# Kernel tuning notes

Hardware: AMD Instinct MI355X
Metric: run time of the kernel (lower is better)

Reference implementation:

```python
import jax, jax.numpy as jnp
import numpy as np

EMB = 768
HEADS = 12
HD = EMB // HEADS
FF = 4 * EMB
EPS = 1e-5


def gelu_tanh(x):
    c = jnp.sqrt(jnp.asarray(2.0 / jnp.pi, x.dtype))
    return 0.5 * x * (1.0 + jnp.tanh(c * (x + 0.044715 * x ** 3)))


def layernorm(x, scale, shift):
    mean = x.mean(-1, keepdims=True)
    var = ((x - mean) ** 2).mean(-1, keepdims=True)
    return scale * (x - mean) / jnp.sqrt(var + EPS) + shift


def setup_inputs() -> dict:
    key = jax.random.key(0)
    ks = jax.random.split(key, 12)
    s = 0.02
    return {
        "x": jax.random.normal(ks[0], (8, 1024, EMB), jnp.float32),
        "Wq": jax.random.normal(ks[1], (EMB, EMB), jnp.float32) * s,
        "Wk": jax.random.normal(ks[2], (EMB, EMB), jnp.float32) * s,
        "Wv": jax.random.normal(ks[3], (EMB, EMB), jnp.float32) * s,
        "Wo": jax.random.normal(ks[4], (EMB, EMB), jnp.float32) * s,
        "bo": jnp.zeros((EMB,), jnp.float32),
        "W1": jax.random.normal(ks[5], (EMB, FF), jnp.float32) * s,
        "b1": jnp.zeros((FF,), jnp.float32),
        "W2": jax.random.normal(ks[6], (FF, EMB), jnp.float32) * s,
        "b2": jnp.zeros((EMB,), jnp.float32),
        "ln1_scale": jnp.ones((EMB,), jnp.float32),
        "ln1_shift": jnp.zeros((EMB,), jnp.float32),
        "ln2_scale": jnp.ones((EMB,), jnp.float32),
        "ln2_shift": jnp.zeros((EMB,), jnp.float32),
    }


def reference(x, Wq, Wk, Wv, Wo, bo, W1, b1, W2, b2,
              ln1_scale, ln1_shift, ln2_scale, ln2_shift):
    B, T, _ = x.shape
    inp = x
    h = layernorm(x, ln1_scale, ln1_shift)
    # QKV projections (no bias, qkv_bias=False)
    q = (h @ Wq).reshape(B, T, HEADS, HD).transpose(0, 2, 1, 3)  # [B,H,T,hd]
    k = (h @ Wk).reshape(B, T, HEADS, HD).transpose(0, 2, 1, 3)
    v = (h @ Wv).reshape(B, T, HEADS, HD).transpose(0, 2, 1, 3)
    scores = jnp.einsum('bhqd,bhkd->bhqk', q, k)
    causal = jnp.triu(jnp.ones((T, T), bool), k=1)
    scores = jnp.where(causal, -jnp.inf, scores)
    attn = jax.nn.softmax(scores / jnp.sqrt(jnp.asarray(HD, x.dtype)), axis=-1)
    ctx = jnp.einsum('bhqk,bhkd->bhqd', attn, v)
    ctx = ctx.transpose(0, 2, 1, 3).reshape(B, T, EMB)
    attn_out = ctx @ Wo + bo
    x = inp + attn_out  # dropout is identity (rate 0 / eval)
    inp = x
    h = layernorm(x, ln2_scale, ln2_shift)
    ff = gelu_tanh(h @ W1 + b1) @ W2 + b2
    return inp + ff
```

## Files before the change

kernel.cpp:

```cpp
#include <hip/hip_runtime.h>
#include <hip/hip_bf16.h>
#include <stdint.h>
#include <stddef.h>

#define EMB 768
#define FFD 3072
#define NHEAD 12
#define HD 64
#define SEQ 1024
#define NTOK 8192
#define QKVW 2304

typedef unsigned short u16;
typedef __attribute__((ext_vector_type(8))) short short8;
typedef __attribute__((ext_vector_type(4))) float f32x4;

__device__ __forceinline__ u16 f2bf(float f) {
  union { float f; uint32_t u; } w; w.f = f;
  uint32_t x = w.u + 0x7fffu + ((w.u >> 16) & 1u);
  return (u16)(x >> 16);
}

__device__ __forceinline__ float bf2f(uint32_t v) {
  union { uint32_t u; float f; } c; c.u = v << 16; return c.f;
}

__device__ __forceinline__ uint32_t pkbf(float lo, float hi) {
  __hip_bfloat162 h = __float22bfloat162_rn(float2{lo, hi});
  union { __hip_bfloat162 h; uint32_t u; } cv; cv.h = h;
  return cv.u;
}

__device__ __forceinline__ void g2l16(const void* g, void* l) {
  __builtin_amdgcn_global_load_lds(
      (const __attribute__((address_space(1))) void*)g,
      (__attribute__((address_space(3))) void*)l, 16, 0, 0);
}

__global__ __launch_bounds__(256)
void prep_kernel(const float* __restrict__ Wq, const float* __restrict__ Wk,
                 const float* __restrict__ Wv, const float* __restrict__ Wo,
                 const float* __restrict__ W1, const float* __restrict__ W2,
                 u16* __restrict__ qkvT, u16* __restrict__ woT,
                 u16* __restrict__ w1T, u16* __restrict__ w2T,
                 const float* __restrict__ x, const float* __restrict__ sc,
                 const float* __restrict__ sh, u16* __restrict__ h1) {
  __shared__ float tile[32][33];
  const int id = blockIdx.x;
  if (id >= 6912) {
    const int wave = threadIdx.x >> 6, lane = threadIdx.x & 63;
    const int row = (id - 6912) * 4 + wave;
    const float* xr = x + (size_t)row * EMB;
    float4 v[3];
    float s = 0.f, ss = 0.f;
#pragma unroll
    for (int i = 0; i < 3; ++i) {
      v[i] = *(const float4*)(xr + lane * 4 + i * 256);
      s += v[i].x + v[i].y + v[i].z + v[i].w;
      ss += v[i].x * v[i].x + v[i].y * v[i].y + v[i].z * v[i].z + v[i].w * v[i].w;
    }
#pragma unroll
    for (int m = 1; m < 64; m <<= 1) { s += __shfl_xor(s, m, 64); ss += __shfl_xor(ss, m, 64); }
    const float mean = s * (1.f / EMB);
    const float inv = rsqrtf(ss * (1.f / EMB) - mean * mean + 1e-5f);
    u16* orow = h1 + (size_t)row * EMB;
#pragma unroll
    for (int i = 0; i < 3; ++i) {
      const int c = lane * 4 + i * 256;
      const float4 s4 = *(const float4*)(sc + c);
      const float4 h4 = *(const float4*)(sh + c);
      uint2 w2;
      w2.x = pkbf((v[i].x - mean) * inv * s4.x + h4.x, (v[i].y - mean) * inv * s4.y + h4.y);
      w2.y = pkbf((v[i].z - mean) * inv * s4.z + h4.z, (v[i].w - mean) * inv * s4.w + h4.w);
      *(uint2*)(orow + c) = w2;
    }
    return;
  }
  const float* in; u16* out; int K, N, bx, by;
  if (id < 1728) {
    const int z = id / 576, rem = id % 576;
    in = z == 0 ? Wq : (z == 1 ? Wk : Wv);
    out = qkvT + (size_t)z * EMB * EMB;
    K = EMB; N = EMB; bx = rem % 24; by = rem / 24;
  } else if (id < 2304) {
    const int rem = id - 1728;
    in = Wo; out = woT; K = EMB; N = EMB; bx = rem % 24; by = rem / 24;
  } else if (id < 4608) {
    const int rem = id - 2304;
    in = W1; out = w1T; K = EMB; N = FFD; bx = rem % 96; by = rem / 96;
  } else {
    const int rem = id - 4608;
    in = W2; out = w2T; K = FFD; N = EMB; bx = rem % 24; by = rem / 24;
  }
  const int n0 = bx * 32, k0 = by * 32;
  const int tx = threadIdx.x & 31;
  const int ty = threadIdx.x >> 5;
#pragma unroll
  for (int i = 0; i < 32; i += 8)
    tile[ty + i][tx] = in[(size_t)(k0 + ty + i) * N + n0 + tx];
  __syncthreads();
#pragma unroll
  for (int i = 0; i < 32; i += 8)
    out[(size_t)(n0 + ty + i) * K + k0 + tx] = f2bf(tile[tx][ty + i]);
}

__global__ __launch_bounds__(256)
void ln_bf_vec_kernel(const u16* __restrict__ x, const float* __restrict__ sc,
                      const float* __restrict__ sh, u16* __restrict__ out) {
  const int wave = threadIdx.x >> 6, lane = threadIdx.x & 63;
  const int row = blockIdx.x * 4 + wave;
  const u16* xr = x + (size_t)row * EMB;
  float v[3][4];
  float s = 0.f, ss = 0.f;
#pragma unroll
  for (int i = 0; i < 3; ++i) {
    const uint2 r2 = *(const uint2*)(xr + lane * 4 + i * 256);
    v[i][0] = bf2f(r2.x & 0xffffu);
    v[i][1] = bf2f(r2.x >> 16);
    v[i][2] = bf2f(r2.y & 0xffffu);
    v[i][3] = bf2f(r2.y >> 16);
#pragma unroll
    for (int j = 0; j < 4; ++j) { s += v[i][j]; ss += v[i][j] * v[i][j]; }
  }
#pragma unroll
  for (int m = 1; m < 64; m <<= 1) { s += __shfl_xor(s, m, 64); ss += __shfl_xor(ss, m, 64); }
  const float mean = s * (1.f / EMB);
  const float inv = rsqrtf(ss * (1.f / EMB) - mean * mean + 1e-5f);
  u16* orow = out + (size_t)row * EMB;
#pragma unroll
  for (int i = 0; i < 3; ++i) {
    const int c = lane * 4 + i * 256;
    const float4 s4 = *(const float4*)(sc + c);
    const float4 h4 = *(const float4*)(sh + c);
    uint2 w2;
    w2.x = pkbf((v[i][0] - mean) * inv * s4.x + h4.x, (v[i][1] - mean) * inv * s4.y + h4.y);
    w2.y = pkbf((v[i][2] - mean) * inv * s4.z + h4.z, (v[i][3] - mean) * inv * s4.w + h4.w);
    *(uint2*)(orow + c) = w2;
  }
}

template <int EPI, int MT, bool SWAP>
__global__ __launch_bounds__(256, 4)
void gemm_kernel(const u16* __restrict__ A, const u16* __restrict__ BT,
                 void* __restrict__ Cp, const float* __restrict__ bias,
                 const float* __restrict__ res, const u16* __restrict__ res16,
                 u16* __restrict__ vTp, int M, int N, int K) {
  constexpr int MI = MT / 32;
  __shared__ u16 As[MT * 64];
  __shared__ u16 Bs[128 * 64];

  const int nwg = gridDim.x * gridDim.y;
  const int orig = blockIdx.y * gridDim.x + blockIdx.x;
  const int swz = (orig & 7) * (nwg >> 3) + (orig >> 3);
  const int m0 = (swz % gridDim.y) * MT;
  const int n0 = (swz / gridDim.y) * 128;

  const int tid = threadIdx.x;
  const int wave = tid >> 6, lane = tid & 63;
  const int wr = wave >> 1, wc = wave & 1;
  const int r = lane & 15, g = lane >> 4;
  const int lrow = lane >> 3;
  const int lelem = (lane & 7) * 8;

  f32x4 acc[MI][4] = {};

  const int nkt = K >> 6;
  for (int kt = 0; kt < nkt; ++kt) {
    const int k0 = kt << 6;
    if (kt) __syncthreads();
#pragma unroll
    for (int q = 0; q < MT / 32; ++q) {
      const int chunk = q * 4 + wave;
      const int row = chunk * 8 + lrow;
      const int e = lelem ^ ((row & 7) << 3);
      g2l16(A + (size_t)(m0 + row) * K + k0 + e, As + chunk * 512);
    }
#pragma unroll
    for (int q = 0; q < 4; ++q) {
      const int chunk = q * 4 + wave;
      const int row = chunk * 8 + lrow;
      const int e = lelem ^ ((row & 7) << 3);
      g2l16(BT + (size_t)(n0 + row) * K + k0 + e, Bs + chunk * 512);
    }
    __syncthreads();
#pragma unroll
    for (int kk = 0; kk < 2; ++kk) {
      short8 af[MI], bf[4];
#pragma unroll
      for (int mi = 0; mi < MI; ++mi) {
        const int row = wr * (MT / 2) + mi * 16 + r;
        af[mi] = *(const short8*)(As + row * 64 + ((kk * 32 + g * 8) ^ ((row & 7) << 3)));
      }
#pragma unroll
      for (int ni = 0; ni < 4; ++ni) {
        const int row = wc * 64 + ni * 16 + r;
        bf[ni] = *(const short8*)(Bs + row * 64 + ((kk * 32 + g * 8) ^ ((row & 7) << 3)));
      }
#pragma unroll
      for (int mi = 0; mi < MI; ++mi)
#pragma unroll
        for (int ni = 0; ni < 4; ++ni) {
          if constexpr (SWAP)
            acc[mi][ni] = __builtin_amdgcn_mfma_f32_16x16x32_bf16(bf[ni], af[mi], acc[mi][ni], 0, 0, 0);
          else
            acc[mi][ni] = __builtin_amdgcn_mfma_f32_16x16x32_bf16(af[mi], bf[ni], acc[mi][ni], 0, 0, 0);
        }
    }
  }

  if constexpr (!SWAP) {
#pragma unroll
    for (int mi = 0; mi < MI; ++mi)
#pragma unroll
      for (int ni = 0; ni < 4; ++ni) {
        const int rowb = m0 + wr * (MT / 2) + mi * 16 + 4 * g;
        const int col = n0 + wc * 64 + ni * 16 + r;
        u16 pk[4];
#pragma unroll
        for (int j = 0; j < 4; ++j) pk[j] = f2bf(acc[mi][ni][j]);
        if (col < 1536) {
#pragma unroll
          for (int j = 0; j < 4; ++j)
            ((u16*)Cp)[(size_t)(rowb + j) * N + col] = pk[j];
        } else {
          uint2 w2;
          w2.x = (uint32_t)pk[0] | ((uint32_t)pk[1] << 16);
          w2.y = (uint32_t)pk[2] | ((uint32_t)pk[3] << 16);
          *(uint2*)(vTp + (size_t)(col - 1536) * NTOK + rowb) = w2;
        }
      }
  } else {
#pragma unroll
    for (int mi = 0; mi < MI; ++mi) {
      const int m = m0 + wr * (MT / 2) + mi * 16 + r;
#pragma unroll
      for (int ni = 0; ni < 4; ++ni) {
        const int nb = n0 + wc * 64 + ni * 16 + 4 * g;
        if constexpr (EPI == 2) {
          const float4 bs = *(const float4*)(bias + nb);
          float tj[4];
#pragma unroll
          for (int j = 0; j < 4; ++j) {
            float t = acc[mi][ni][j] + (&bs.x)[j];
            float e = __expf(1.5957691216057308f * (t + 0.044715f * t * t * t));
            tj[j] = 0.5f * t * (1.f + (1.f - 2.f / (e + 1.f)));
          }
          uint2 w2;
          w2.x = pkbf(tj[0], tj[1]);
          w2.y = pkbf(tj[2], tj[3]);
          *(uint2*)((u16*)Cp + (size_t)m * N + nb) = w2;
        } else if constexpr (EPI == 4) {
          const float4 bs = *(const float4*)(bias + nb);
          const float4 rs = *(const float4*)(res + (size_t)m * N + nb);
          uint2 w2;
          w2.x = pkbf(acc[mi][ni][0] + bs.x + rs.x, acc[mi][ni][1] + bs.y + rs.y);
          w2.y = pkbf(acc[mi][ni][2] + bs.z + rs.z, acc[mi][ni][3] + bs.w + rs.w);
          *(uint2*)((u16*)Cp + (size_t)m * N + nb) = w2;
        } else {
          const float4 bs = *(const float4*)(bias + nb);
          const uint2 r2 = *(const uint2*)(res16 + (size_t)m * N + nb);
          float4 o;
          o.x = acc[mi][ni][0] + bs.x + bf2f(r2.x & 0xffffu);
          o.y = acc[mi][ni][1] + bs.y + bf2f(r2.x >> 16);
          o.z = acc[mi][ni][2] + bs.z + bf2f(r2.y & 0xffffu);
          o.w = acc[mi][ni][3] + bs.w + bf2f(r2.y >> 16);
          *(float4*)((float*)Cp + (size_t)m * N + nb) = o;
        }
      }
    }
  }
}

#define CEXP 0.18033688011112042f

__global__ __launch_bounds__(256, 3)
void attn_kernel(const u16* __restrict__ qkv, const u16* __restrict__ vT,
                 u16* __restrict__ ctx) {
  const int bh = blockIdx.x;
  const int qt = blockIdx.y;
  const int b = bh / NHEAD, h = bh % NHEAD;
  const int tid = threadIdx.x;
  const int wave = tid >> 6, lane = tid & 63;
  const int r = lane & 15, g = lane >> 4;

  __shared__ u16 Kb[2][64 * 64];
  __shared__ u16 Vb[2][64 * 64];
  __shared__ u16 Pt[4][16 * 64];

  const int qw = qt * 128 + wave * 32;
  const int tok0 = b * SEQ;

  short8 aq[2][2];
#pragma unroll
  for (int qf = 0; qf < 2; ++qf) {
    const u16* qb = qkv + (size_t)(tok0 + qw + qf * 16 + r) * QKVW + h * HD;
    aq[qf][0] = *(const short8*)(qb + g * 8);
    aq[qf][1] = *(const short8*)(qb + 32 + g * 8);
  }

  float l_st[2] = {0.f, 0.f};
  f32x4 oc[2][4] = {};

  const int sr = tid >> 3;
  const int sc = (tid & 7) * 8;
  const int nt = 2 * qt + 2;

  const u16* kg = qkv + (size_t)tok0 * QKVW + EMB + h * HD;
  const u16* vg = vT + (size_t)(h * HD) * NTOK + tok0;
  const int e0 = sc ^ ((sr & 7) << 3);

  auto stage = [&](int buf, int kt) {
    const size_t koff = (size_t)kt * 64;
    u16* kb = (u16*)Kb[buf] + wave * 512;
    u16* vb = (u16*)Vb[buf] + wave * 512;
    g2l16(kg + (koff + sr) * QKVW + e0, kb);
    g2l16(kg + (koff + sr + 32) * QKVW + e0, kb + 2048);
    g2l16(vg + (size_t)sr * NTOK + koff + e0, vb);
    g2l16(vg + (size_t)(sr + 32) * NTOK + koff + e0, vb + 2048);
  };

  stage(0, 0);
  for (int kb = 0; kb < nt; ++kb) {
    __syncthreads();
    const int cur = kb & 1;
    if (kb + 1 < nt) stage(cur ^ 1, kb + 1);

    const int kv0 = kb * 64;
    if (kv0 > qw + 31) continue;

    short8 kf[4][2];
#pragma unroll
    for (int nf = 0; nf < 4; ++nf) {
      const int row = nf * 16 + r;
#pragma unroll
      for (int kk = 0; kk < 2; ++kk)
        kf[nf][kk] = *(const short8*)((char*)Kb[cur] + row * 128 +
                                      ((kk * 64 + g * 16) ^ ((row & 7) << 4)));
    }
    short8 bv[2][4];
#pragma unroll
    for (int half = 0; half < 2; ++half)
#pragma unroll
      for (int nd = 0; nd < 4; ++nd) {
        const int vr = nd * 16 + r;
        bv[half][nd] = *(const short8*)((char*)Vb[cur] + vr * 128 +
                       ((half * 64 + g * 16) ^ ((vr & 7) << 4)));
      }

#pragma unroll
    for (int qf = 0; qf < 2; ++qf) {
      f32x4 st[4];
#pragma unroll
      for (int nf = 0; nf < 4; ++nf) {
        f32x4 z = {};
        z = __builtin_amdgcn_mfma_f32_16x16x32_bf16(kf[nf][0], aq[qf][0], z, 0, 0, 0);
        z = __builtin_amdgcn_mfma_f32_16x16x32_bf16(kf[nf][1], aq[qf][1], z, 0, 0, 0);
        st[nf] = z;
      }
      if (kv0 + 63 > qw + qf * 16) {
        const int qg = qw + qf * 16 + r;
#pragma unroll
        for (int nf = 0; nf < 4; ++nf)
#pragma unroll
          for (int j = 0; j < 4; ++j)
            if (kv0 + nf * 16 + 4 * g + j > qg) st[nf][j] = -3e38f;
      }
      float p[4][4];
      float ps = 0.f;
#pragma unroll
      for (int nf = 0; nf < 4; ++nf)
#pragma unroll
        for (int j = 0; j < 4; ++j) {
          const float pe = exp2f(st[nf][j] * CEXP);
          p[nf][j] = pe;
          ps += pe;
        }
      ps += __shfl_xor(ps, 16);
      ps += __shfl_xor(ps, 32);
      l_st[qf] += ps;

      u16* Pw = (u16*)Pt[wave];
#pragma unroll
      for (int nf = 0; nf < 4; ++nf) {
        uint2 w2;
        w2.x = pkbf(p[nf][0], p[nf][1]);
        w2.y = pkbf(p[nf][2], p[nf][3]);
        *(uint2*)((char*)Pw + r * 128 + ((nf * 32 + g * 8) ^ ((r & 7) << 4))) = w2;
      }
#pragma unroll
      for (int half = 0; half < 2; ++half) {
        short8 pa = *(const short8*)((char*)Pw + r * 128 +
                                     ((half * 64 + g * 16) ^ ((r & 7) << 4)));
#pragma unroll
        for (int nd = 0; nd < 4; ++nd)
          oc[qf][nd] = __builtin_amdgcn_mfma_f32_16x16x32_bf16(pa, bv[half][nd], oc[qf][nd], 0, 0, 0);
      }
    }
  }

#pragma unroll
  for (int qf = 0; qf < 2; ++qf) {
    const float rl = 1.f / l_st[qf];
#pragma unroll
    for (int j = 0; j < 4; ++j) {
      const float rj = __shfl(rl, 4 * g + j, 16);
      const size_t row = (size_t)tok0 + qw + qf * 16 + 4 * g + j;
#pragma unroll
      for (int nd = 0; nd < 4; ++nd)
        ctx[row * EMB + h * HD + nd * 16 + r] = f2bf(oc[qf][nd][j] * rj);
    }
  }
}

extern "C" void kernel_launch(void* const* d_in, const int* in_sizes, int n_in,
                              void* d_out, int out_size, void* d_ws, size_t ws_size,
                              hipStream_t stream) {
  const float* x    = (const float*)d_in[0];
  const float* Wq   = (const float*)d_in[1];
  const float* Wk   = (const float*)d_in[2];
  const float* Wv   = (const float*)d_in[3];
  const float* Wo   = (const float*)d_in[4];
  const float* bo   = (const float*)d_in[5];
  const float* W1   = (const float*)d_in[6];
  const float* b1   = (const float*)d_in[7];
  const float* W2   = (const float*)d_in[8];
  const float* b2   = (const float*)d_in[9];
  const float* ln1s = (const float*)d_in[10];
  const float* ln1b = (const float*)d_in[11];
  const float* ln2s = (const float*)d_in[12];
  const float* ln2b = (const float*)d_in[13];

  char* p = (char*)d_ws;
  u16* qkvT = (u16*)p; p += (size_t)QKVW * EMB * 2;
  u16* woT  = (u16*)p; p += (size_t)EMB * EMB * 2;
  u16* w1T  = (u16*)p; p += (size_t)FFD * EMB * 2;
  u16* w2T  = (u16*)p; p += (size_t)EMB * FFD * 2;
  u16* h1   = (u16*)p; p += (size_t)NTOK * EMB * 2;
  u16* qkv  = (u16*)p; p += (size_t)NTOK * QKVW * 2;
  u16* x2bf = (u16*)p; p += (size_t)NTOK * EMB * 2;
  u16* ff1  = (u16*)p; p += (size_t)NTOK * FFD * 2;
  u16* ctxb = h1;
  u16* h2   = qkv;
  u16* vT   = ff1;

  if (ws_size < (size_t)(p - (char*)d_ws)) return;

  dim3 blk(256);
  prep_kernel<<<8960, blk, 0, stream>>>(Wq, Wk, Wv, Wo, W1, W2, qkvT, woT, w1T, w2T,
                                        x, ln1s, ln1b, h1);
  gemm_kernel<3, 128, false><<<dim3(18, 64), blk, 0, stream>>>(h1, qkvT, qkv, nullptr, nullptr, nullptr, vT, NTOK, QKVW, EMB);
  attn_kernel<<<dim3(96, 8), blk, 0, stream>>>(qkv, vT, ctxb);
  gemm_kernel<4, 64, true><<<dim3(6, 128), blk, 0, stream>>>(ctxb, woT, x2bf, bo, x, nullptr, nullptr, NTOK, EMB, EMB);
  ln_bf_vec_kernel<<<NTOK / 4, blk, 0, stream>>>(x2bf, ln2s, ln2b, h2);
  gemm_kernel<2, 128, true><<<dim3(24, 64), blk, 0, stream>>>(h2, w1T, ff1, b1, nullptr, nullptr, nullptr, NTOK, FFD, EMB);
  gemm_kernel<5, 64, true><<<dim3(6, 128), blk, 0, stream>>>(ff1, w2T, (float*)d_out, b2, nullptr, x2bf, nullptr, NTOK, EMB, FFD);
}
```

Measured before the change: 260.5 us.

## Split QKV GEMM into vectorized Q/K and transposed-V kernels, retune tile order

The fused QKV projection is split into two launches. The Q/K part now uses the swapped MFMA operand order so each lane writes packed 4-element row-major bf16 stores, replacing the old scattered 2-byte stores. The V part is a separate GEMM that writes only the transposed V buffer. Separately, the occupancy hint in launch bounds is removed and the tile swizzle now walks N-fastest instead of M-fastest, which changes register allocation and L2 reuse for every GEMM. The cost is one extra kernel launch plus a second read of the LN1 activations.

```diff
diff --git a/kernel.cpp b/kernel.cpp
--- a/kernel.cpp
+++ b/kernel.cpp
@@ -140,7 +140,7 @@
 }
 
 template <int EPI, int MT, bool SWAP>
-__global__ __launch_bounds__(256, 4)
+__global__ __launch_bounds__(256)
 void gemm_kernel(const u16* __restrict__ A, const u16* __restrict__ BT,
                  void* __restrict__ Cp, const float* __restrict__ bias,
                  const float* __restrict__ res, const u16* __restrict__ res16,
@@ -152,8 +152,8 @@
   const int nwg = gridDim.x * gridDim.y;
   const int orig = blockIdx.y * gridDim.x + blockIdx.x;
   const int swz = (orig & 7) * (nwg >> 3) + (orig >> 3);
-  const int m0 = (swz % gridDim.y) * MT;
-  const int n0 = (swz / gridDim.y) * 128;
+  const int m0 = (swz / gridDim.x) * MT;
+  const int n0 = (swz % gridDim.x) * 128;
 
   const int tid = threadIdx.x;
   const int wave = tid >> 6, lane = tid & 63;
@@ -215,19 +215,10 @@
       for (int ni = 0; ni < 4; ++ni) {
         const int rowb = m0 + wr * (MT / 2) + mi * 16 + 4 * g;
         const int col = n0 + wc * 64 + ni * 16 + r;
-        u16 pk[4];
-#pragma unroll
-        for (int j = 0; j < 4; ++j) pk[j] = f2bf(acc[mi][ni][j]);
-        if (col < 1536) {
-#pragma unroll
-          for (int j = 0; j < 4; ++j)
-            ((u16*)Cp)[(size_t)(rowb + j) * N + col] = pk[j];
-        } else {
-          uint2 w2;
-          w2.x = (uint32_t)pk[0] | ((uint32_t)pk[1] << 16);
-          w2.y = (uint32_t)pk[2] | ((uint32_t)pk[3] << 16);
-          *(uint2*)(vTp + (size_t)(col - 1536) * NTOK + rowb) = w2;
-        }
+        uint2 w2;
+        w2.x = pkbf(acc[mi][ni][0], acc[mi][ni][1]);
+        w2.y = pkbf(acc[mi][ni][2], acc[mi][ni][3]);
+        *(uint2*)(vTp + (size_t)col * NTOK + rowb) = w2;
       }
   } else {
 #pragma unroll
@@ -256,7 +247,7 @@
           w2.x = pkbf(acc[mi][ni][0] + bs.x + rs.x, acc[mi][ni][1] + bs.y + rs.y);
           w2.y = pkbf(acc[mi][ni][2] + bs.z + rs.z, acc[mi][ni][3] + bs.w + rs.w);
           *(uint2*)((u16*)Cp + (size_t)m * N + nb) = w2;
-        } else {
+        } else if constexpr (EPI == 5) {
           const float4 bs = *(const float4*)(bias + nb);
           const uint2 r2 = *(const uint2*)(res16 + (size_t)m * N + nb);
           float4 o;
@@ -265,6 +256,11 @@
           o.z = acc[mi][ni][2] + bs.z + bf2f(r2.y & 0xffffu);
           o.w = acc[mi][ni][3] + bs.w + bf2f(r2.y >> 16);
           *(float4*)((float*)Cp + (size_t)m * N + nb) = o;
+        } else {
+          uint2 w2;
+          w2.x = pkbf(acc[mi][ni][0], acc[mi][ni][1]);
+          w2.y = pkbf(acc[mi][ni][2], acc[mi][ni][3]);
+          *(uint2*)((u16*)Cp + (size_t)m * N + nb) = w2;
         }
       }
     }
@@ -448,7 +444,10 @@
   dim3 blk(256);
   prep_kernel<<<8960, blk, 0, stream>>>(Wq, Wk, Wv, Wo, W1, W2, qkvT, woT, w1T, w2T,
                                         x, ln1s, ln1b, h1);
-  gemm_kernel<3, 128, false><<<dim3(18, 64), blk, 0, stream>>>(h1, qkvT, qkv, nullptr, nullptr, nullptr, vT, NTOK, QKVW, EMB);
+  gemm_kernel<6, 128, true><<<dim3(12, 64), blk, 0, stream>>>(
+      h1, qkvT, qkv, nullptr, nullptr, nullptr, nullptr, NTOK, QKVW, EMB);
+  gemm_kernel<7, 128, false><<<dim3(6, 64), blk, 0, stream>>>(
+      h1, qkvT + (size_t)1536 * EMB, nullptr, nullptr, nullptr, nullptr, vT, NTOK, EMB, EMB);
   attn_kernel<<<dim3(96, 8), blk, 0, stream>>>(qkv, vT, ctxb);
   gemm_kernel<4, 64, true><<<dim3(6, 128), blk, 0, stream>>>(ctxb, woT, x2bf, bo, x, nullptr, nullptr, NTOK, EMB, EMB);
   ln_bf_vec_kernel<<<NTOK / 4, blk, 0, stream>>>(x2bf, ln2s, ln2b, h2);
```

Measured after the change: 226.4 us. -13.1%, faster.
